# Optimization experiments

Hardware: AMD Instinct MI355X
Metric: run time of the kernel (lower is better)

Reference implementation:

```python
import jax, jax.numpy as jnp
import numpy as np

B = 64          # decode batch (num_tokens, q_len=1 each)
HIDDEN = 4096
NH = 32         # query heads
NKV = 8         # kv heads (GQA)
HD = 128        # head_dim = hidden/NH
S = 2048        # max cached context per sequence
BLOCK = 16      # paged-cache block size
NBLK = B * (S // BLOCK)  # 8192 physical blocks
THETA = 10000.0


def _rope(x, positions):
    # x: [B, H, D] -- neox-style (half-split) llama RoPE
    d = x.shape[-1]
    inv_freq = 1.0 / (THETA ** (jnp.arange(0, d, 2, dtype=jnp.float32) / d))  # [D/2]
    ang = positions.astype(jnp.float32)[:, None] * inv_freq[None, :]          # [B, D/2]
    cos = jnp.cos(ang)[:, None, :]
    sin = jnp.sin(ang)[:, None, :]
    x1, x2 = jnp.split(x, 2, axis=-1)
    return jnp.concatenate([x1 * cos - x2 * sin, x2 * cos + x1 * sin], axis=-1)


def setup_inputs() -> dict:
    key = jax.random.key(0)
    ks = jax.random.split(key, 10)
    hidden_states = jax.random.randint(ks[0], (B, HIDDEN), -128, 128, dtype=jnp.int32).astype(jnp.int8)
    w_qkv = jax.random.randint(ks[1], (HIDDEN, (NH + 2 * NKV) * HD), -128, 128, dtype=jnp.int32).astype(jnp.int8)
    w_o = jax.random.randint(ks[2], (NH * HD, HIDDEN), -128, 128, dtype=jnp.int32).astype(jnp.int8)
    k_cache = jax.random.randint(ks[3], (NBLK, BLOCK, NKV, HD), -128, 128, dtype=jnp.int32).astype(jnp.int8)
    v_cache = jax.random.randint(ks[4], (NBLK, BLOCK, NKV, HD), -128, 128, dtype=jnp.int32).astype(jnp.int8)
    block_tables = jnp.arange(NBLK, dtype=jnp.int32).reshape(B, S // BLOCK)
    context_lens = jax.random.randint(ks[5], (B,), 256, S, dtype=jnp.int32)
    positions = context_lens  # new token appended at index context_len
    q_scale = jax.random.uniform(ks[6], (), minval=0.005, maxval=0.02, dtype=jnp.float32)
    k_scale = jax.random.uniform(ks[7], (), minval=0.005, maxval=0.02, dtype=jnp.float32)
    v_scale = jax.random.uniform(ks[8], (), minval=0.005, maxval=0.02, dtype=jnp.float32)
    o_scale = jax.random.uniform(ks[9], (), minval=0.005, maxval=0.02, dtype=jnp.float32)
    return dict(positions=positions, hidden_states=hidden_states, w_qkv=w_qkv, w_o=w_o,
                k_cache=k_cache, v_cache=v_cache, block_tables=block_tables,
                context_lens=context_lens, q_scale=q_scale, k_scale=k_scale,
                v_scale=v_scale, o_scale=o_scale)


def reference(positions, hidden_states, w_qkv, w_o, k_cache, v_cache,
              block_tables, context_lens, q_scale, k_scale, v_scale, o_scale):
    scaling = HD ** -0.5
    q_size, kv_size = NH * HD, NKV * HD
    qkv = jnp.matmul(hidden_states.astype(jnp.int32), w_qkv.astype(jnp.int32))  # [B, 6144]
    # fused dequant + RoPE
    q = qkv[:, :q_size].astype(jnp.float32).reshape(B, NH, HD) * q_scale
    k = qkv[:, q_size:q_size + kv_size].astype(jnp.float32).reshape(B, NKV, HD) * k_scale
    v = qkv[:, q_size + kv_size:].astype(jnp.float32).reshape(B, NKV, HD) * v_scale
    q = _rope(q, positions)
    k = _rope(k, positions)
    # paged-cache gather + dequant: [B, n_blk, BLOCK, NKV, HD] -> [B, S, NKV, HD]
    K = (k_cache[block_tables].astype(jnp.float32) * k_scale).reshape(B, S, NKV, HD)
    V = (v_cache[block_tables].astype(jnp.float32) * v_scale).reshape(B, S, NKV, HD)
    # append current token's k/v (as the cache write would)
    K = jnp.concatenate([K, k[:, None]], axis=1)  # [B, S+1, NKV, HD]
    V = jnp.concatenate([V, v[:, None]], axis=1)
    idx = jnp.arange(S + 1)
    valid = (idx[None, :] < context_lens[:, None]) | (idx[None, :] == S)  # [B, S+1]
    # GQA: group query heads over kv heads
    qg = q.reshape(B, NKV, NH // NKV, HD)
    scores = jnp.einsum('bhgd,bshd->bhgs', qg, K) * scaling  # [B, NKV, G, S+1]
    scores = jnp.where(valid[:, None, None, :], scores, jnp.float32(-1e30))
    p = jax.nn.softmax(scores, axis=-1)
    attn = jnp.einsum('bhgs,bshd->bhgd', p, V).reshape(B, NH * HD)
    # quantized o_proj with dequant scale
    out = jnp.matmul(attn, w_o.astype(jnp.float32)) * o_scale  # [B, HIDDEN]
    return out
```

## Files before the change

### kernel.cpp

```cpp
#include <hip/hip_runtime.h>

typedef int   v4i  __attribute__((ext_vector_type(4)));
typedef short bf8  __attribute__((ext_vector_type(8)));
typedef float f32x4 __attribute__((ext_vector_type(4)));

#define B_   64
#define HIDDEN_ 4096
#define NH_  32
#define NKV_ 8
#define HD_  128
#define S_   2048
#define NQKV 6144
#define CHUNK 256
#define NCHUNK 8
#define KSPLIT 8
#define QKV_PART (64 * NQKV)

__device__ __forceinline__ unsigned pack_i8(int a, int b, int c, int d) {
    return (a & 0xff) | ((b & 0xff) << 8) | ((c & 0xff) << 16) | (d << 24);
}

__global__ __launch_bounds__(256) void qkv_gemm(const int* __restrict__ A,
                                                const int* __restrict__ W,
                                                int* __restrict__ Cp) {
    __shared__ signed char Wl[2][64 * 80];
    const int tid = threadIdx.x;
    const int n0  = blockIdx.x * 64;
    const int ky  = blockIdx.y;
    const int kbeg = ky * (HIDDEN_ / KSPLIT);
    const int wv  = tid >> 6;
    const int l   = tid & 63;
    const int lr  = l & 15;
    const int lk  = l >> 4;
    const int sn  = tid & 63;
    const int sk  = (tid >> 6) * 16;

    const int* Wg = W + (long)(kbeg + sk) * NQKV + n0 + sn;

    v4i acc[4] = {v4i{0,0,0,0}, v4i{0,0,0,0}, v4i{0,0,0,0}, v4i{0,0,0,0}};
    int rA[16], rB[16];

#define LOADW(R, CH) { const int* wp = Wg + (long)(CH) * 64 * NQKV;              \
    _Pragma("unroll") for (int j = 0; j < 16; ++j) R[j] = wp[j * NQKV]; }
#define STAGEW(R, BUF) { unsigned d0 = pack_i8(R[0],R[1],R[2],R[3]);             \
    unsigned d1 = pack_i8(R[4],R[5],R[6],R[7]);                                  \
    unsigned d2 = pack_i8(R[8],R[9],R[10],R[11]);                                \
    unsigned d3 = pack_i8(R[12],R[13],R[14],R[15]);                              \
    v4i t = {(int)d0,(int)d1,(int)d2,(int)d3};                                   \
    *(v4i*)&Wl[BUF][sn * 80 + sk] = t; }
#define COMPW(BUF, CH) { const int* ap = A + (long)(wv*16+lr)*HIDDEN_ + kbeg + (CH)*64 + lk*16; \
    unsigned av[4];                                                              \
    _Pragma("unroll") for (int j = 0; j < 4; ++j) {                              \
        int4 t = *(const int4*)(ap + 4*j); av[j] = pack_i8(t.x,t.y,t.z,t.w); }   \
    v4i a = *(v4i*)av;                                                           \
    _Pragma("unroll") for (int nt = 0; nt < 4; ++nt) {                           \
        v4i bb = *(const v4i*)&Wl[BUF][(nt*16+lr)*80 + lk*16];                   \
        acc[nt] = __builtin_amdgcn_mfma_i32_16x16x64_i8(a, bb, acc[nt], 0,0,0); } }

    LOADW(rA, 0);
#pragma unroll 1
    for (int ch = 0; ch < 8; ch += 2) {
        STAGEW(rA, 0);
        LOADW(rB, ch + 1);
        __syncthreads();
        COMPW(0, ch);
        STAGEW(rB, 1);
        if (ch < 6) LOADW(rA, ch + 2);
        __syncthreads();
        COMPW(1, ch + 1);
    }
    int* Co = Cp + (long)ky * QKV_PART;
#pragma unroll
    for (int nt = 0; nt < 4; ++nt)
#pragma unroll
        for (int r = 0; r < 4; ++r) {
            int m = wv * 16 + (l >> 4) * 4 + r;
            int n = n0 + nt * 16 + (l & 15);
            Co[m * NQKV + n] = acc[nt][r];
        }
#undef LOADW
#undef STAGEW
#undef COMPW
}

__device__ __forceinline__ float rd8(const int* __restrict__ q, int idx) {
    int v = 0;
#pragma unroll
    for (int p = 0; p < KSPLIT; ++p) v += q[p * QKV_PART + idx];
    return (float)v;
}

__global__ __launch_bounds__(256) void rope_dequant(const int* __restrict__ qkvp,
                                                    const int* __restrict__ positions,
                                                    const float* qs_p, const float* ks_p,
                                                    const float* vs_p,
                                                    float* __restrict__ qf,
                                                    float* __restrict__ knew,
                                                    float* __restrict__ vnew) {
    const int b = blockIdx.x, part = blockIdx.y;
    const int tid = threadIdx.x;
    __shared__ float cs[64], sn[64];
    const float qs = qs_p[0], ks = ks_p[0], vs = vs_p[0];
    if (tid < 64) {
        float invf = 1.0f / powf(10000.0f, (float)tid * (1.0f / 64.0f));
        float ang  = (float)positions[b] * invf;
        cs[tid] = cosf(ang);
        sn[tid] = sinf(ang);
    }
    __syncthreads();
    const int base = b * NQKV;
    if (part < 2) {
        for (int t = tid; t < 1024; t += 256) {
            int head = part * 16 + (t >> 6), i = t & 63;
            float x1 = rd8(qkvp, base + head * 128 + i) * qs;
            float x2 = rd8(qkvp, base + head * 128 + 64 + i) * qs;
            float c = cs[i], s = sn[i];
            qf[(b * NH_ + head) * 128 + i]      = x1 * c - x2 * s;
            qf[(b * NH_ + head) * 128 + 64 + i] = x2 * c + x1 * s;
        }
    } else if (part == 2) {
        for (int t = tid; t < 512; t += 256) {
            int h = t >> 6, i = t & 63;
            float x1 = rd8(qkvp, base + 4096 + h * 128 + i) * ks;
            float x2 = rd8(qkvp, base + 4096 + h * 128 + 64 + i) * ks;
            float c = cs[i], s = sn[i];
            knew[(b * NKV_ + h) * 128 + i]      = x1 * c - x2 * s;
            knew[(b * NKV_ + h) * 128 + 64 + i] = x2 * c + x1 * s;
        }
    } else {
        for (int t = tid; t < 1024; t += 256) {
            int h = t >> 7, d = t & 127;
            vnew[(b * NKV_ + h) * 128 + d] = rd8(qkvp, base + 5120 + h * 128 + d) * vs;
        }
    }
}

__global__ __launch_bounds__(256) void attn_decode(const int* __restrict__ kc,
                                                   const int* __restrict__ vc,
                                                   const int* __restrict__ btab,
                                                   const int* __restrict__ ctx_lens,
                                                   const float* __restrict__ qf,
                                                   const float* ks_p, const float* vs_p,
                                                   float* __restrict__ po,
                                                   float* __restrict__ pm,
                                                   float* __restrict__ pl) {
    const int c  = blockIdx.x;
    const int bh = blockIdx.y;
    const int b = bh >> 3, h = bh & 7;
    const int ctx = ctx_lens[b];
    const int s0g = c * CHUNK;
    const int n = min(ctx - s0g, CHUNK);
    if (n <= 0) return;

    __shared__ float sc[4][264];
    __shared__ float opart[512][9];
    __shared__ int   bts[CHUNK / 16];

    const int tid = threadIdx.x;
    const int wv  = tid >> 6;
    const int l   = tid & 63;
    const int tok = l >> 4;
    const int dq  = l & 15;

    if (tid < CHUNK / 16) bts[tid] = btab[b * 128 + (s0g >> 4) + tid];

    const float kss = ks_p[0] * 0.08838834764831845f;
    const float vscale = vs_p[0];

    float qr[4][8];
#pragma unroll
    for (int g = 0; g < 4; ++g) {
        const float* qp = qf + (long)(b * NH_ + h * 4 + g) * 128 + dq * 8;
        float4 v0 = *(const float4*)(qp);
        float4 v1 = *(const float4*)(qp + 4);
        qr[g][0]=v0.x; qr[g][1]=v0.y; qr[g][2]=v0.z; qr[g][3]=v0.w;
        qr[g][4]=v1.x; qr[g][5]=v1.y; qr[g][6]=v1.z; qr[g][7]=v1.w;
    }
    __syncthreads();

    {
        const int nsweep = (n + 15) >> 4;
        int srel = wv * 4 + tok;
        int4 w0, w1;
        {
            int seff = min(srel, n - 1);
            int blk = bts[seff >> 4];
            const int* kp = kc + (long)(blk * 16 + (seff & 15)) * 1024 + h * 128 + dq * 8;
            w0 = *(const int4*)kp;
            w1 = *(const int4*)(kp + 4);
        }
#pragma unroll 1
        for (int it = 0; it < nsweep; ++it) {
            int4 u0, u1;
            const bool more = (it + 1 < nsweep);
            if (more) {
                int snx = min(srel + 16, n - 1);
                int blk = bts[snx >> 4];
                const int* kp = kc + (long)(blk * 16 + (snx & 15)) * 1024 + h * 128 + dq * 8;
                u0 = *(const int4*)kp;
                u1 = *(const int4*)(kp + 4);
            }
            float kf[8];
            kf[0]=(float)w0.x; kf[1]=(float)w0.y; kf[2]=(float)w0.z; kf[3]=(float)w0.w;
            kf[4]=(float)w1.x; kf[5]=(float)w1.y; kf[6]=(float)w1.z; kf[7]=(float)w1.w;
            float p0 = 0.f, p1 = 0.f, p2 = 0.f, p3 = 0.f;
#pragma unroll
            for (int j = 0; j < 8; ++j) {
                p0 += qr[0][j] * kf[j];
                p1 += qr[1][j] * kf[j];
                p2 += qr[2][j] * kf[j];
                p3 += qr[3][j] * kf[j];
            }
#pragma unroll
            for (int off = 1; off < 16; off <<= 1) {
                p0 += __shfl_xor(p0, off, 16);
                p1 += __shfl_xor(p1, off, 16);
                p2 += __shfl_xor(p2, off, 16);
                p3 += __shfl_xor(p3, off, 16);
            }
            if (srel < n && dq < 4) {
                float psel = (dq == 0) ? p0 : (dq == 1) ? p1 : (dq == 2) ? p2 : p3;
                sc[dq][srel] = psel * kss;
            }
            if (more) { w0 = u0; w1 = u1; }
            srel += 16;
        }
    }
    __syncthreads();

    {
        float m = -1e30f;
        for (int s = l; s < n; s += 64) m = fmaxf(m, sc[wv][s]);
#pragma unroll
        for (int off = 1; off < 64; off <<= 1) m = fmaxf(m, __shfl_xor(m, off, 64));
        float sum = 0.f;
        for (int s = l; s < n; s += 64) {
            float e = __expf(sc[wv][s] - m);
            sc[wv][s] = e;
            sum += e;
        }
#pragma unroll
        for (int off = 1; off < 64; off <<= 1) sum += __shfl_xor(sum, off, 64);
        if (l == 0) {
            int idx = (c * 512 + bh) * 4 + wv;
            pm[idx] = m;
            pl[idx] = sum;
        }
    }
    __syncthreads();

    const int d4 = tid & 31;
    const int sp = tid >> 5;
    float acc[4][4] = {};
    int s = sp;
#pragma unroll 1
    for (; s + 56 < n; s += 64) {
        int4 w[8];
#pragma unroll
        for (int j = 0; j < 8; ++j) {
            int ss = s + 8 * j;
            int blk = bts[ss >> 4];
            w[j] = *(const int4*)(vc + (long)(blk * 16 + (ss & 15)) * 1024 + h * 128 + d4 * 4);
        }
#pragma unroll
        for (int j = 0; j < 8; ++j) {
            int ss = s + 8 * j;
            float v0 = (float)w[j].x, v1 = (float)w[j].y, v2 = (float)w[j].z, v3 = (float)w[j].w;
#pragma unroll
            for (int g = 0; g < 4; ++g) {
                float p = sc[g][ss];
                acc[g][0] += p * v0; acc[g][1] += p * v1;
                acc[g][2] += p * v2; acc[g][3] += p * v3;
            }
        }
    }
#pragma unroll 1
    for (; s < n; s += 8) {
        int blk = bts[s >> 4];
        int4 w = *(const int4*)(vc + (long)(blk * 16 + (s & 15)) * 1024 + h * 128 + d4 * 4);
        float v0 = (float)w.x, v1 = (float)w.y, v2 = (float)w.z, v3 = (float)w.w;
#pragma unroll
        for (int g = 0; g < 4; ++g) {
            float p = sc[g][s];
            acc[g][0] += p * v0; acc[g][1] += p * v1;
            acc[g][2] += p * v2; acc[g][3] += p * v3;
        }
    }
#pragma unroll
    for (int g = 0; g < 4; ++g)
#pragma unroll
        for (int j = 0; j < 4; ++j)
            opart[g * 128 + d4 * 4 + j][sp] = acc[g][j];
    __syncthreads();

    for (int oi = tid; oi < 512; oi += 256) {
        float o = 0.f;
#pragma unroll
        for (int p = 0; p < 8; ++p) o += opart[oi][p];
        po[(long)((c * 512 + bh) * 4 + (oi >> 7)) * 128 + (oi & 127)] = o * vscale;
    }
}

__global__ __launch_bounds__(256) void attn_merge(const float* __restrict__ qf,
                                                  const float* __restrict__ knew,
                                                  const float* __restrict__ vnew,
                                                  const int* __restrict__ ctx_lens,
                                                  const float* __restrict__ po,
                                                  const float* __restrict__ pm,
                                                  const float* __restrict__ pl,
                                                  unsigned short* __restrict__ attn) {
    const int bh = blockIdx.x;
    const int b = bh >> 3, h = bh & 7;
    const int ctx = ctx_lens[b];
    const int nc = (ctx + CHUNK - 1) / CHUNK;
    const int tid = threadIdx.x;
    const int wv = tid >> 6, l = tid & 63;
    __shared__ float snew_s[4];

    {
        const float* kn = knew + (b * NKV_ + h) * 128;
        const float* qp = qf + (long)(b * NH_ + h * 4 + wv) * 128;
        float p = qp[l] * kn[l] + qp[l + 64] * kn[l + 64];
#pragma unroll
        for (int off = 1; off < 64; off <<= 1) p += __shfl_xor(p, off, 64);
        if (l == 0) snew_s[wv] = p * 0.08838834764831845f;
    }
    __syncthreads();

    for (int oi = tid; oi < 512; oi += 256) {
        int g = oi >> 7, d = oi & 127;
        float snew = snew_s[g];
        float M = snew;
        for (int c = 0; c < nc; ++c)
            M = fmaxf(M, pm[(c * 512 + bh) * 4 + g]);
        float wn = __expf(snew - M);
        float L = wn;
        float O = wn * vnew[(b * NKV_ + h) * 128 + d];
        for (int c = 0; c < nc; ++c) {
            float w = __expf(pm[(c * 512 + bh) * 4 + g] - M);
            L += pl[(c * 512 + bh) * 4 + g] * w;
            O += po[(long)((c * 512 + bh) * 4 + g) * 128 + d] * w;
        }
        float res = O / L;
        unsigned int u = __float_as_uint(res);
        unsigned int r = (u + 0x7fffu + ((u >> 16) & 1u)) >> 16;
        attn[b * 4096 + (h * 4 + g) * 128 + d] = (unsigned short)r;
    }
}

__global__ __launch_bounds__(256) void oproj(const unsigned short* __restrict__ Abf,
                                             const int* __restrict__ W,
                                             const float* os_p,
                                             float* __restrict__ out) {
    __shared__ unsigned short Wl[4][16 * 72];
    const int tid = threadIdx.x;
    const int n0  = blockIdx.x * 16;
    const int wv  = tid >> 6, l = tid & 63;
    const int lr  = l & 15, lk = l >> 4;
    const float osc = os_p[0];
    const int sn  = tid & 15;
    const int sk4 = (tid >> 4) * 4;

    const int* Wg = W + (long)sk4 * HIDDEN_ + n0 + sn;

    f32x4 acc = f32x4{0.f, 0.f, 0.f, 0.f};
    int r0[4], r1[4], r2[4], r3[4];

#define LOADO(R, CH) { const int* wp = Wg + (long)(CH) * 64 * HIDDEN_;           \
    _Pragma("unroll") for (int j = 0; j < 4; ++j) R[j] = wp[j * HIDDEN_]; }
#define STAGEO(R, BUF) { ushort4 hb;                                             \
    hb.x = (unsigned short)(__float_as_uint((float)R[0]) >> 16);                 \
    hb.y = (unsigned short)(__float_as_uint((float)R[1]) >> 16);                 \
    hb.z = (unsigned short)(__float_as_uint((float)R[2]) >> 16);                 \
    hb.w = (unsigned short)(__float_as_uint((float)R[3]) >> 16);                 \
    *(ushort4*)&Wl[BUF][sn * 72 + sk4] = hb; }
#define COMPO(BUF, CH) { _Pragma("unroll") for (int kh = 0; kh < 2; ++kh) {      \
    bf8 a = *(const bf8*)(Abf + (long)(wv*16+lr)*HIDDEN_ + (CH)*64 + kh*32 + lk*8); \
    bf8 bb = *(const bf8*)&Wl[BUF][lr * 72 + kh * 32 + lk * 8];                  \
    acc = __builtin_amdgcn_mfma_f32_16x16x32_bf16(a, bb, acc, 0, 0, 0); } }

    LOADO(r0, 0); LOADO(r1, 1); LOADO(r2, 2); LOADO(r3, 3);
#pragma unroll 1
    for (int ch = 0; ch < 64; ch += 4) {
        STAGEO(r0, 0); STAGEO(r1, 1); STAGEO(r2, 2); STAGEO(r3, 3);
        __syncthreads();
        if (ch < 60) { LOADO(r0, ch+4); LOADO(r1, ch+5); LOADO(r2, ch+6); LOADO(r3, ch+7); }
        COMPO(0, ch); COMPO(1, ch+1); COMPO(2, ch+2); COMPO(3, ch+3);
        __syncthreads();
    }
#pragma unroll
    for (int r = 0; r < 4; ++r) {
        int m = wv * 16 + (l >> 4) * 4 + r;
        int n = n0 + (l & 15);
        out[m * HIDDEN_ + n] = acc[r] * osc;
    }
#undef LOADO
#undef STAGEO
#undef COMPO
}

extern "C" void kernel_launch(void* const* d_in, const int* in_sizes, int n_in,
                              void* d_out, int out_size, void* d_ws, size_t ws_size,
                              hipStream_t stream) {
    const int*   positions = (const int*)d_in[0];
    const int*   hidden    = (const int*)d_in[1];
    const int*   w_qkv     = (const int*)d_in[2];
    const int*   w_o       = (const int*)d_in[3];
    const int*   kcache    = (const int*)d_in[4];
    const int*   vcache    = (const int*)d_in[5];
    const int*   btab      = (const int*)d_in[6];
    const int*   ctxl      = (const int*)d_in[7];
    const float* qs        = (const float*)d_in[8];
    const float* ks        = (const float*)d_in[9];
    const float* vs        = (const float*)d_in[10];
    const float* os        = (const float*)d_in[11];

    char* ws = (char*)d_ws;
    int*            qkvp  = (int*)ws;
    float*          po    = (float*)ws;
    float*          qf    = (float*)(ws + 16777216);
    float*          knew  = (float*)(ws + 17825792);
    float*          vnew  = (float*)(ws + 18087936);
    unsigned short* attnb = (unsigned short*)(ws + 18350080);
    float*          pm    = (float*)(ws + 18874368);
    float*          pl    = (float*)(ws + 19005440);

    qkv_gemm<<<dim3(NQKV / 64, KSPLIT), 256, 0, stream>>>(hidden, w_qkv, qkvp);
    rope_dequant<<<dim3(B_, 4), 256, 0, stream>>>(qkvp, positions, qs, ks, vs, qf, knew, vnew);
    attn_decode<<<dim3(NCHUNK, B_ * NKV_), 256, 0, stream>>>(kcache, vcache, btab, ctxl,
                                                             qf, ks, vs, po, pm, pl);
    attn_merge<<<B_ * NKV_, 256, 0, stream>>>(qf, knew, vnew, ctxl, po, pm, pl, attnb);
    oproj<<<HIDDEN_ / 16, 256, 0, stream>>>(attnb, w_o, os, (float*)d_out);
}
```

Before: 233.5 us.

## Prefetch V alongside K into packed int8 LDS and halve attention chunk size

The attention kernel now loads V rows together with K rows in the score loop, packs them to int8 and stages them in shared memory. The PV accumulation then reads V from LDS instead of issuing a second round of global loads after the softmax. CHUNK drops from 256 to 128 and NCHUNK rises to 16, which doubles the number of blocks so the extra LDS per block still fits and parallelism improves. The trade-off is more register pressure from the doubled prefetch, more LDS use, and more partial results for the combine step to merge.

```diff
diff --git a/kernel.cpp b/kernel.cpp
--- a/kernel.cpp
+++ b/kernel.cpp
@@ -11,8 +11,8 @@
 #define HD_  128
 #define S_   2048
 #define NQKV 6144
-#define CHUNK 256
-#define NCHUNK 8
+#define CHUNK 128
+#define NCHUNK 16
 #define KSPLIT 8
 #define QKV_PART (64 * NQKV)
 
@@ -152,7 +152,8 @@
     const int n = min(ctx - s0g, CHUNK);
     if (n <= 0) return;
 
-    __shared__ float sc[4][264];
+    __shared__ float sc[4][132];
+    __shared__ unsigned Vl8[CHUNK][32];
     __shared__ float opart[512][9];
     __shared__ int   bts[CHUNK / 16];
 
@@ -181,28 +182,26 @@
     {
         const int nsweep = (n + 15) >> 4;
         int srel = wv * 4 + tok;
-        int4 w0, w1;
+        int4 kA, kB, vA, vB;
         {
             int seff = min(srel, n - 1);
-            int blk = bts[seff >> 4];
-            const int* kp = kc + (long)(blk * 16 + (seff & 15)) * 1024 + h * 128 + dq * 8;
-            w0 = *(const int4*)kp;
-            w1 = *(const int4*)(kp + 4);
+            long off = (long)(bts[seff >> 4] * 16 + (seff & 15)) * 1024 + h * 128 + dq * 8;
+            kA = *(const int4*)(kc + off); kB = *(const int4*)(kc + off + 4);
+            vA = *(const int4*)(vc + off); vB = *(const int4*)(vc + off + 4);
         }
 #pragma unroll 1
         for (int it = 0; it < nsweep; ++it) {
-            int4 u0, u1;
+            int4 ukA, ukB, uvA, uvB;
             const bool more = (it + 1 < nsweep);
             if (more) {
                 int snx = min(srel + 16, n - 1);
-                int blk = bts[snx >> 4];
-                const int* kp = kc + (long)(blk * 16 + (snx & 15)) * 1024 + h * 128 + dq * 8;
-                u0 = *(const int4*)kp;
-                u1 = *(const int4*)(kp + 4);
+                long off = (long)(bts[snx >> 4] * 16 + (snx & 15)) * 1024 + h * 128 + dq * 8;
+                ukA = *(const int4*)(kc + off); ukB = *(const int4*)(kc + off + 4);
+                uvA = *(const int4*)(vc + off); uvB = *(const int4*)(vc + off + 4);
             }
             float kf[8];
-            kf[0]=(float)w0.x; kf[1]=(float)w0.y; kf[2]=(float)w0.z; kf[3]=(float)w0.w;
-            kf[4]=(float)w1.x; kf[5]=(float)w1.y; kf[6]=(float)w1.z; kf[7]=(float)w1.w;
+            kf[0]=(float)kA.x; kf[1]=(float)kA.y; kf[2]=(float)kA.z; kf[3]=(float)kA.w;
+            kf[4]=(float)kB.x; kf[5]=(float)kB.y; kf[6]=(float)kB.z; kf[7]=(float)kB.w;
             float p0 = 0.f, p1 = 0.f, p2 = 0.f, p3 = 0.f;
 #pragma unroll
             for (int j = 0; j < 8; ++j) {
@@ -218,11 +217,17 @@
                 p2 += __shfl_xor(p2, off, 16);
                 p3 += __shfl_xor(p3, off, 16);
             }
-            if (srel < n && dq < 4) {
-                float psel = (dq == 0) ? p0 : (dq == 1) ? p1 : (dq == 2) ? p2 : p3;
-                sc[dq][srel] = psel * kss;
+            if (srel < n) {
+                if (dq < 4) {
+                    float psel = (dq == 0) ? p0 : (dq == 1) ? p1 : (dq == 2) ? p2 : p3;
+                    sc[dq][srel] = psel * kss;
+                }
+                uint2 t;
+                t.x = pack_i8(vA.x, vA.y, vA.z, vA.w);
+                t.y = pack_i8(vB.x, vB.y, vB.z, vB.w);
+                *(uint2*)&Vl8[srel][dq * 2] = t;
             }
-            if (more) { w0 = u0; w1 = u1; }
+            if (more) { kA = ukA; kB = ukB; vA = uvA; vB = uvB; }
             srel += 16;
         }
     }
@@ -252,33 +257,13 @@
     const int d4 = tid & 31;
     const int sp = tid >> 5;
     float acc[4][4] = {};
-    int s = sp;
-#pragma unroll 1
-    for (; s + 56 < n; s += 64) {
-        int4 w[8];
-#pragma unroll
-        for (int j = 0; j < 8; ++j) {
-            int ss = s + 8 * j;
-            int blk = bts[ss >> 4];
-            w[j] = *(const int4*)(vc + (long)(blk * 16 + (ss & 15)) * 1024 + h * 128 + d4 * 4);
-        }
-#pragma unroll
-        for (int j = 0; j < 8; ++j) {
-            int ss = s + 8 * j;
-            float v0 = (float)w[j].x, v1 = (float)w[j].y, v2 = (float)w[j].z, v3 = (float)w[j].w;
-#pragma unroll
-            for (int g = 0; g < 4; ++g) {
-                float p = sc[g][ss];
-                acc[g][0] += p * v0; acc[g][1] += p * v1;
-                acc[g][2] += p * v2; acc[g][3] += p * v3;
-            }
-        }
-    }
-#pragma unroll 1
-    for (; s < n; s += 8) {
-        int blk = bts[s >> 4];
-        int4 w = *(const int4*)(vc + (long)(blk * 16 + (s & 15)) * 1024 + h * 128 + d4 * 4);
-        float v0 = (float)w.x, v1 = (float)w.y, v2 = (float)w.z, v3 = (float)w.w;
+#pragma unroll 4
+    for (int s = sp; s < n; s += 8) {
+        unsigned w = Vl8[s][d4];
+        float v0 = (float)(int)(signed char)(w & 0xff);
+        float v1 = (float)(int)(signed char)((w >> 8) & 0xff);
+        float v2 = (float)(int)(signed char)((w >> 16) & 0xff);
+        float v3 = (float)(int)(signed char)(w >> 24);
 #pragma unroll
         for (int g = 0; g < 4; ++g) {
             float p = sc[g][s];
```

Result: slower. 246.4 us (+5.5%).

## Split-K o_proj GEMM with 64-wide tiles and batch K-cache loads four per thread

Applied to the files above, without the earlier changes.

The o_proj kernel moves from 256 blocks of 16 columns over the full K to a 64x16 grid of 64-column tiles, each covering K/16. Partial results go to workspace and a new reduce kernel sums them and applies the output scale. Separately, the attention score loop now has each thread group issue four K-cache row loads at once per sweep, replacing the one-ahead software prefetch, to raise memory-level parallelism. The cost is an extra launch, a 16 MB partial buffer that is written and read back, and higher register use in both kernels.

```diff
diff --git a/kernel.cpp b/kernel.cpp
--- a/kernel.cpp
+++ b/kernel.cpp
@@ -14,7 +14,9 @@
 #define CHUNK 256
 #define NCHUNK 8
 #define KSPLIT 8
+#define OSPLIT 16
 #define QKV_PART (64 * NQKV)
+#define OPROJ_PART (64 * HIDDEN_)
 
 __device__ __forceinline__ unsigned pack_i8(int a, int b, int c, int d) {
     return (a & 0xff) | ((b & 0xff) << 8) | ((c & 0xff) << 16) | (d << 24);
@@ -179,51 +181,46 @@
     __syncthreads();
 
     {
-        const int nsweep = (n + 15) >> 4;
-        int srel = wv * 4 + tok;
-        int4 w0, w1;
-        {
-            int seff = min(srel, n - 1);
-            int blk = bts[seff >> 4];
-            const int* kp = kc + (long)(blk * 16 + (seff & 15)) * 1024 + h * 128 + dq * 8;
-            w0 = *(const int4*)kp;
-            w1 = *(const int4*)(kp + 4);
-        }
+        const int grp = wv * 4 + tok;
+        const int nsweep = (n + 63) >> 6;
+        int base = grp * 4;
 #pragma unroll 1
         for (int it = 0; it < nsweep; ++it) {
-            int4 u0, u1;
-            const bool more = (it + 1 < nsweep);
-            if (more) {
-                int snx = min(srel + 16, n - 1);
-                int blk = bts[snx >> 4];
-                const int* kp = kc + (long)(blk * 16 + (snx & 15)) * 1024 + h * 128 + dq * 8;
-                u0 = *(const int4*)kp;
-                u1 = *(const int4*)(kp + 4);
+            int4 wA[4], wB[4];
+#pragma unroll
+            for (int t = 0; t < 4; ++t) {
+                int seff = min(base + t, n - 1);
+                long off = (long)(bts[seff >> 4] * 16 + (seff & 15)) * 1024 + h * 128 + dq * 8;
+                wA[t] = *(const int4*)(kc + off);
+                wB[t] = *(const int4*)(kc + off + 4);
             }
-            float kf[8];
-            kf[0]=(float)w0.x; kf[1]=(float)w0.y; kf[2]=(float)w0.z; kf[3]=(float)w0.w;
-            kf[4]=(float)w1.x; kf[5]=(float)w1.y; kf[6]=(float)w1.z; kf[7]=(float)w1.w;
-            float p0 = 0.f, p1 = 0.f, p2 = 0.f, p3 = 0.f;
-#pragma unroll
-            for (int j = 0; j < 8; ++j) {
-                p0 += qr[0][j] * kf[j];
-                p1 += qr[1][j] * kf[j];
-                p2 += qr[2][j] * kf[j];
-                p3 += qr[3][j] * kf[j];
+#pragma unroll
+            for (int t = 0; t < 4; ++t) {
+                float kf[8];
+                kf[0]=(float)wA[t].x; kf[1]=(float)wA[t].y; kf[2]=(float)wA[t].z; kf[3]=(float)wA[t].w;
+                kf[4]=(float)wB[t].x; kf[5]=(float)wB[t].y; kf[6]=(float)wB[t].z; kf[7]=(float)wB[t].w;
+                float p0 = 0.f, p1 = 0.f, p2 = 0.f, p3 = 0.f;
+#pragma unroll
+                for (int j = 0; j < 8; ++j) {
+                    p0 += qr[0][j] * kf[j];
+                    p1 += qr[1][j] * kf[j];
+                    p2 += qr[2][j] * kf[j];
+                    p3 += qr[3][j] * kf[j];
+                }
+#pragma unroll
+                for (int off = 1; off < 16; off <<= 1) {
+                    p0 += __shfl_xor(p0, off, 16);
+                    p1 += __shfl_xor(p1, off, 16);
+                    p2 += __shfl_xor(p2, off, 16);
+                    p3 += __shfl_xor(p3, off, 16);
+                }
+                int srel = base + t;
+                if (srel < n && dq < 4) {
+                    float psel = (dq == 0) ? p0 : (dq == 1) ? p1 : (dq == 2) ? p2 : p3;
+                    sc[dq][srel] = psel * kss;
+                }
             }
-#pragma unroll
-            for (int off = 1; off < 16; off <<= 1) {
-                p0 += __shfl_xor(p0, off, 16);
-                p1 += __shfl_xor(p1, off, 16);
-                p2 += __shfl_xor(p2, off, 16);
-                p3 += __shfl_xor(p3, off, 16);
-            }
-            if (srel < n && dq < 4) {
-                float psel = (dq == 0) ? p0 : (dq == 1) ? p1 : (dq == 2) ? p2 : p3;
-                sc[dq][srel] = psel * kss;
-            }
-            if (more) { w0 = u0; w1 = u1; }
-            srel += 16;
+            base += 64;
         }
     }
     __syncthreads();
@@ -348,55 +345,73 @@
     }
 }
 
-__global__ __launch_bounds__(256) void oproj(const unsigned short* __restrict__ Abf,
-                                             const int* __restrict__ W,
-                                             const float* os_p,
-                                             float* __restrict__ out) {
-    __shared__ unsigned short Wl[4][16 * 72];
+__global__ __launch_bounds__(256) void oproj_gemm(const unsigned short* __restrict__ Abf,
+                                                  const int* __restrict__ W,
+                                                  float* __restrict__ Cp) {
+    __shared__ unsigned short Wl[2][64 * 72];
     const int tid = threadIdx.x;
-    const int n0  = blockIdx.x * 16;
-    const int wv  = tid >> 6, l = tid & 63;
-    const int lr  = l & 15, lk = l >> 4;
-    const float osc = os_p[0];
-    const int sn  = tid & 15;
-    const int sk4 = (tid >> 4) * 4;
-
-    const int* Wg = W + (long)sk4 * HIDDEN_ + n0 + sn;
-
-    f32x4 acc = f32x4{0.f, 0.f, 0.f, 0.f};
-    int r0[4], r1[4], r2[4], r3[4];
+    const int n0  = blockIdx.x * 64;
+    const int ky  = blockIdx.y;
+    const int kbeg = ky * (HIDDEN_ / OSPLIT);
+    const int wv  = tid >> 6;
+    const int l   = tid & 63;
+    const int lr  = l & 15;
+    const int lk  = l >> 4;
+    const int sn  = tid & 63;
+    const int sk  = (tid >> 6) * 16;
+
+    const int* Wg = W + (long)(kbeg + sk) * HIDDEN_ + n0 + sn;
+
+    f32x4 acc[4] = {f32x4{0,0,0,0}, f32x4{0,0,0,0}, f32x4{0,0,0,0}, f32x4{0,0,0,0}};
+    int rA[16], rB[16];
 
 #define LOADO(R, CH) { const int* wp = Wg + (long)(CH) * 64 * HIDDEN_;           \
-    _Pragma("unroll") for (int j = 0; j < 4; ++j) R[j] = wp[j * HIDDEN_]; }
-#define STAGEO(R, BUF) { ushort4 hb;                                             \
-    hb.x = (unsigned short)(__float_as_uint((float)R[0]) >> 16);                 \
-    hb.y = (unsigned short)(__float_as_uint((float)R[1]) >> 16);                 \
-    hb.z = (unsigned short)(__float_as_uint((float)R[2]) >> 16);                 \
-    hb.w = (unsigned short)(__float_as_uint((float)R[3]) >> 16);                 \
-    *(ushort4*)&Wl[BUF][sn * 72 + sk4] = hb; }
+    _Pragma("unroll") for (int j = 0; j < 16; ++j) R[j] = wp[j * HIDDEN_]; }
+#define STAGEO(R, BUF) { unsigned short hb[16];                                  \
+    _Pragma("unroll") for (int j = 0; j < 16; ++j)                               \
+        hb[j] = (unsigned short)(__float_as_uint((float)R[j]) >> 16);            \
+    *(v4i*)&Wl[BUF][sn * 72 + sk]     = *(v4i*)&hb[0];                           \
+    *(v4i*)&Wl[BUF][sn * 72 + sk + 8] = *(v4i*)&hb[8]; }
 #define COMPO(BUF, CH) { _Pragma("unroll") for (int kh = 0; kh < 2; ++kh) {      \
-    bf8 a = *(const bf8*)(Abf + (long)(wv*16+lr)*HIDDEN_ + (CH)*64 + kh*32 + lk*8); \
-    bf8 bb = *(const bf8*)&Wl[BUF][lr * 72 + kh * 32 + lk * 8];                  \
-    acc = __builtin_amdgcn_mfma_f32_16x16x32_bf16(a, bb, acc, 0, 0, 0); } }
-
-    LOADO(r0, 0); LOADO(r1, 1); LOADO(r2, 2); LOADO(r3, 3);
+    bf8 a = *(const bf8*)(Abf + (long)(wv*16+lr)*HIDDEN_ + kbeg + (CH)*64 + kh*32 + lk*8); \
+    _Pragma("unroll") for (int nt = 0; nt < 4; ++nt) {                           \
+        bf8 bb = *(const bf8*)&Wl[BUF][(nt*16+lr)*72 + kh*32 + lk*8];            \
+        acc[nt] = __builtin_amdgcn_mfma_f32_16x16x32_bf16(a, bb, acc[nt], 0,0,0); } } }
+
+    LOADO(rA, 0);
 #pragma unroll 1
-    for (int ch = 0; ch < 64; ch += 4) {
-        STAGEO(r0, 0); STAGEO(r1, 1); STAGEO(r2, 2); STAGEO(r3, 3);
+    for (int ch = 0; ch < 4; ch += 2) {
+        STAGEO(rA, 0);
+        LOADO(rB, ch + 1);
         __syncthreads();
-        if (ch < 60) { LOADO(r0, ch+4); LOADO(r1, ch+5); LOADO(r2, ch+6); LOADO(r3, ch+7); }
-        COMPO(0, ch); COMPO(1, ch+1); COMPO(2, ch+2); COMPO(3, ch+3);
+        COMPO(0, ch);
+        STAGEO(rB, 1);
+        if (ch < 2) LOADO(rA, ch + 2);
         __syncthreads();
-    }
-#pragma unroll
-    for (int r = 0; r < 4; ++r) {
-        int m = wv * 16 + (l >> 4) * 4 + r;
-        int n = n0 + (l & 15);
-        out[m * HIDDEN_ + n] = acc[r] * osc;
-    }
+        COMPO(1, ch + 1);
+    }
+    float* Co = Cp + (long)ky * OPROJ_PART;
+#pragma unroll
+    for (int nt = 0; nt < 4; ++nt)
+#pragma unroll
+        for (int r = 0; r < 4; ++r) {
+            int m = wv * 16 + (l >> 4) * 4 + r;
+            int n = n0 + nt * 16 + (l & 15);
+            Co[m * HIDDEN_ + n] = acc[nt][r];
+        }
 #undef LOADO
 #undef STAGEO
 #undef COMPO
+}
+
+__global__ __launch_bounds__(256) void oproj_reduce(const float* __restrict__ Cp,
+                                                    const float* os_p,
+                                                    float* __restrict__ out) {
+    const int i = blockIdx.x * 256 + threadIdx.x;
+    float s = 0.f;
+#pragma unroll
+    for (int p = 0; p < OSPLIT; ++p) s += Cp[(long)p * OPROJ_PART + i];
+    out[i] = s * os_p[0];
 }
 
 extern "C" void kernel_launch(void* const* d_in, const int* in_sizes, int n_in,
@@ -418,6 +433,7 @@
     char* ws = (char*)d_ws;
     int*            qkvp  = (int*)ws;
     float*          po    = (float*)ws;
+    float*          opp   = (float*)ws;
     float*          qf    = (float*)(ws + 16777216);
     float*          knew  = (float*)(ws + 17825792);
     float*          vnew  = (float*)(ws + 18087936);
@@ -430,5 +446,6 @@
     attn_decode<<<dim3(NCHUNK, B_ * NKV_), 256, 0, stream>>>(kcache, vcache, btab, ctxl,
                                                              qf, ks, vs, po, pm, pl);
     attn_merge<<<B_ * NKV_, 256, 0, stream>>>(qf, knew, vnew, ctxl, po, pm, pl, attnb);
-    oproj<<<HIDDEN_ / 16, 256, 0, stream>>>(attnb, w_o, os, (float*)d_out);
-}
+    oproj_gemm<<<dim3(HIDDEN_ / 64, OSPLIT), 256, 0, stream>>>(attnb, w_o, opp);
+    oproj_reduce<<<HIDDEN_ * B_ / 256, 256, 0, stream>>>(opp, os, (float*)d_out);
+}
```

New measurement: 215.7 us (median of 3 runs). -7.6%, faster.
